# Optimization experiments

Hardware: AMD Instinct MI355X
Metric: run time of the kernel (lower is better)

Reference implementation:

```python
import jax, jax.numpy as jnp
import numpy as np

B, N, D = 4, 4096, 768
K_TOP = 8  # module's self.k
EPS = 1e-12  # F.normalize eps


def setup_inputs() -> dict:
    key = jax.random.key(0)
    k0, k1, k2 = jax.random.split(key, 3)
    s = 1.0 / np.sqrt(D)
    feats = jax.random.normal(k0, (B, N, D), dtype=jnp.float32)
    Wq = jax.random.normal(k1, (D, D), dtype=jnp.float32) * s
    bq = jnp.zeros((D,), dtype=jnp.float32)
    Wkv = jax.random.normal(k2, (D, 2 * D), dtype=jnp.float32) * s
    bkv = jnp.zeros((2 * D,), dtype=jnp.float32)
    return {"feats": feats, "Wq": Wq, "bq": bq, "Wkv": Wkv, "bkv": bkv}


def _l2norm(x):
    return x / jnp.maximum(jnp.linalg.norm(x, axis=-1, keepdims=True), EPS)


def reference(feats, Wq, bq, Wkv, bkv):
    # Only self.q and self.kv are used in the original forward; the
    # transformer encoder / norm / score_head / proj are dead code there.
    b, n, d = feats.shape
    Q = feats @ Wq + bq                      # [B,N,D]
    KV = feats @ Wkv + bkv                   # [B,N,2D]
    Kmat, Vmat = jnp.split(KV, 2, axis=-1)   # [B,N,D] each

    # cosine-distance kNN graph (self excluded via +1e6 on diagonal)
    sim = jnp.einsum('bnd,bmd->bnm', _l2norm(Q), _l2norm(Kmat))
    dist = (1.0 - sim) + jnp.eye(n, dtype=sim.dtype)[None] * 1e6
    k_eff = min(n - 1, K_TOP)
    _, idx = jax.lax.top_k(-dist, k_eff)     # smallest distances -> [B,N,k]

    # gather neighbor K/V (no O(N^2 * D) expand)
    bidx = jnp.arange(b)[:, None, None]
    Kn = Kmat[bidx, idx]                     # [B,N,k,D]
    Vn = Vmat[bidx, idx]                     # [B,N,k,D]

    attn = jnp.einsum('bnd,bnkd->bnk', Q, Kn) / np.float32(np.sqrt(d))
    attn = jax.nn.softmax(attn, axis=-1)     # [B,N,k]
    out = jnp.einsum('bnk,bnkd->bnd', attn, Vn)
    return out.mean(axis=1)                  # [B,D]
```

## Files before the change

### kernel.cpp

```cpp
#include <hip/hip_runtime.h>
#include <hip/hip_bf16.h>
#include <math.h>

#define B_ 4
#define N_ 4096
#define D_ 768
#define KTOP 8
#define M_ (B_*N_)
#define TCAND 12
#define SELK 32

typedef __attribute__((ext_vector_type(8))) short short8;
typedef __attribute__((ext_vector_type(4))) float f32x4;
typedef _Float16 half_t;
typedef __attribute__((ext_vector_type(8))) _Float16 half8;
typedef __attribute__((ext_vector_type(4))) _Float16 half4;

__device__ __forceinline__ ushort f2bf(float f) {
    unsigned int u = __float_as_uint(f);
    unsigned int r = (u + 0x7FFFu + ((u >> 16) & 1u)) >> 16;
    return (ushort)r;
}

__device__ __forceinline__ void gload16(const void* g, void* l) {
    __builtin_amdgcn_global_load_lds(
        (const __attribute__((address_space(1))) unsigned int*)g,
        (__attribute__((address_space(3))) unsigned int*)l, 16, 0, 0);
}

__global__ __launch_bounds__(256) void split_feats(
    const float* __restrict__ f, half_t* __restrict__ Fh, half_t* __restrict__ Fl)
{
    const int i = (blockIdx.x * 256 + threadIdx.x) * 4;
    const float4 v = *(const float4*)&f[i];
    float x[4] = {v.x, v.y, v.z, v.w};
    half4 h, l;
#pragma unroll
    for (int c = 0; c < 4; ++c) {
        const half_t hh = (half_t)x[c];
        h[c] = hh;
        l[c] = (half_t)(x[c] - (float)hh);
    }
    *(half4*)&Fh[i] = h;
    *(half4*)&Fl[i] = l;
}

__global__ __launch_bounds__(256) void split_w(
    const float* __restrict__ Wq, const float* __restrict__ Wkv,
    half_t* __restrict__ Wth, half_t* __restrict__ Wtl)
{
    __shared__ float T[64][65];
    const int tid = threadIdx.x;
    const int n0 = blockIdx.x * 64;
    const int k0 = blockIdx.y * 64;

    const int nl = tid & 63;
#pragma unroll
    for (int r = 0; r < 16; ++r) {
        const int kl = (tid >> 6) * 16 + r;
        const int n  = n0 + nl;
        const float w = (n < 768)
            ? Wq[(size_t)(k0 + kl) * 768 + n]
            : Wkv[(size_t)(k0 + kl) * 1536 + (n - 768)];
        T[kl][nl] = w;
    }
    __syncthreads();

    const int kl2 = tid & 63;
#pragma unroll
    for (int r = 0; r < 16; ++r) {
        const int nl2 = (tid >> 6) * 16 + r;
        const float ws = T[kl2][nl2] * 4096.0f;
        const half_t h = (half_t)ws;
        const half_t l = (half_t)(ws - (float)h);
        Wth[(size_t)(n0 + nl2) * D_ + k0 + kl2] = h;
        Wtl[(size_t)(n0 + nl2) * D_ + k0 + kl2] = l;
    }
}

__global__ __launch_bounds__(256) void qkv_mfma(
    const half_t* __restrict__ Fh, const half_t* __restrict__ Fl,
    const half_t* __restrict__ Wth, const half_t* __restrict__ Wtl,
    const float* __restrict__ bq, const float* __restrict__ bkv,
    float* __restrict__ Q, float* __restrict__ Km, float* __restrict__ Vm)
{
    __shared__ __align__(16) half_t Ah[128 * 64];
    __shared__ __align__(16) half_t Al[128 * 64];
    __shared__ __align__(16) half_t Bh[128 * 64];
    __shared__ __align__(16) half_t Bl[128 * 64];

    const int tid  = threadIdx.x;
    const int lane = tid & 63, w = tid >> 6;
    const int wr = w >> 1, wc = w & 1;
    const int r16 = lane & 15, kq = lane >> 4;
    const int n0 = blockIdx.x * 128;
    const int m0 = blockIdx.y * 128;
    const bool three = (n0 < 1536);

    const half_t* ah = Fh  + (size_t)(m0 + (tid >> 3)) * D_ + (tid & 7) * 8;
    const half_t* al = Fl  + (size_t)(m0 + (tid >> 3)) * D_ + (tid & 7) * 8;
    const half_t* bh = Wth + (size_t)(n0 + (tid >> 3)) * D_ + (tid & 7) * 8;
    const half_t* bl = Wtl + (size_t)(n0 + (tid >> 3)) * D_ + (tid & 7) * 8;
    half_t* lAh = Ah + (w << 9);
    half_t* lAl = Al + (w << 9);
    half_t* lBh = Bh + (w << 9);
    half_t* lBl = Bl + (w << 9);

    f32x4 acc[4][4];
#pragma unroll
    for (int mi = 0; mi < 4; ++mi)
#pragma unroll
        for (int ni = 0; ni < 4; ++ni) acc[mi][ni] = (f32x4)0.f;

    for (int kb = 0; kb < D_ / 64; ++kb) {
#pragma unroll
        for (int i = 0; i < 4; ++i) {
            gload16(ah + (size_t)i * 32 * D_ + kb * 64, lAh + i * 2048);
            gload16(bh + (size_t)i * 32 * D_ + kb * 64, lBh + i * 2048);
        }
        if (three) {
#pragma unroll
            for (int i = 0; i < 4; ++i) {
                gload16(al + (size_t)i * 32 * D_ + kb * 64, lAl + i * 2048);
                gload16(bl + (size_t)i * 32 * D_ + kb * 64, lBl + i * 2048);
            }
        }
        __syncthreads();
#pragma unroll
        for (int kk = 0; kk < 2; ++kk) {
            half8 fa[4], fb[4];
#pragma unroll
            for (int mi = 0; mi < 4; ++mi)
                fa[mi] = *(const half8*)&Ah[(wr * 64 + mi * 16 + r16) * 64 + kk * 32 + kq * 8];
#pragma unroll
            for (int ni = 0; ni < 4; ++ni)
                fb[ni] = *(const half8*)&Bh[(wc * 64 + ni * 16 + r16) * 64 + kk * 32 + kq * 8];
#pragma unroll
            for (int mi = 0; mi < 4; ++mi)
#pragma unroll
                for (int ni = 0; ni < 4; ++ni)
                    acc[mi][ni] = __builtin_amdgcn_mfma_f32_16x16x32_f16(
                        fa[mi], fb[ni], acc[mi][ni], 0, 0, 0);
            if (three) {
                half8 gal[4], gbl[4];
#pragma unroll
                for (int mi = 0; mi < 4; ++mi)
                    gal[mi] = *(const half8*)&Al[(wr * 64 + mi * 16 + r16) * 64 + kk * 32 + kq * 8];
#pragma unroll
                for (int ni = 0; ni < 4; ++ni)
                    gbl[ni] = *(const half8*)&Bl[(wc * 64 + ni * 16 + r16) * 64 + kk * 32 + kq * 8];
#pragma unroll
                for (int mi = 0; mi < 4; ++mi)
#pragma unroll
                    for (int ni = 0; ni < 4; ++ni) {
                        acc[mi][ni] = __builtin_amdgcn_mfma_f32_16x16x32_f16(
                            fa[mi], gbl[ni], acc[mi][ni], 0, 0, 0);
                        acc[mi][ni] = __builtin_amdgcn_mfma_f32_16x16x32_f16(
                            gal[mi], fb[ni], acc[mi][ni], 0, 0, 0);
                    }
            }
        }
        __syncthreads();
    }

    const float unscale = 1.0f / 4096.0f;
#pragma unroll
    for (int ni = 0; ni < 4; ++ni) {
        const int n = n0 + wc * 64 + ni * 16 + r16;
        const float bias = (n0 < 768) ? bq[n] : bkv[n - 768];
        float* dst; int nn;
        if      (n0 < 768)  { dst = Q;  nn = n; }
        else if (n0 < 1536) { dst = Km; nn = n - 768; }
        else                { dst = Vm; nn = n - 1536; }
#pragma unroll
        for (int mi = 0; mi < 4; ++mi)
#pragma unroll
            for (int r = 0; r < 4; ++r) {
                const int m = m0 + wr * 64 + mi * 16 + kq * 4 + r;
                dst[(size_t)m * D_ + nn] = acc[mi][ni][r] * unscale + bias;
            }
    }
}

__global__ __launch_bounds__(256) void norm_bf16(
    const float* __restrict__ Q, const float* __restrict__ Km,
    ushort* __restrict__ qn, ushort* __restrict__ kn,
    float* __restrict__ rqinv, float* __restrict__ rkinv)
{
    const int wid  = blockIdx.x * 4 + (threadIdx.x >> 6);
    const int lane = threadIdx.x & 63;
    const float* src; ushort* dst; float* rv; int r;
    if (wid < M_) { src = Q;  dst = qn; rv = rqinv; r = wid; }
    else          { src = Km; dst = kn; rv = rkinv; r = wid - M_; }
    const float* p = src + (size_t)r * D_ + lane * 12;
    float v[12];
#pragma unroll
    for (int i = 0; i < 3; ++i) *(float4*)&v[i * 4] = *(const float4*)&p[i * 4];
    float s = 0.f;
#pragma unroll
    for (int i = 0; i < 12; ++i) s += v[i] * v[i];
#pragma unroll
    for (int off = 32; off; off >>= 1) s += __shfl_xor(s, off);
    const float rinv = 1.0f / fmaxf(sqrtf(s), 1e-12f);
    ushort* op = dst + (size_t)r * D_ + lane * 12;
#pragma unroll
    for (int i = 0; i < 3; ++i) {
        ushort4 o;
        o.x = f2bf(v[i * 4 + 0] * rinv); o.y = f2bf(v[i * 4 + 1] * rinv);
        o.z = f2bf(v[i * 4 + 2] * rinv); o.w = f2bf(v[i * 4 + 3] * rinv);
        *(ushort4*)&op[i * 4] = o;
    }
    if (lane == 0) rv[r] = rinv;
}

__global__ __launch_bounds__(256) void sim_topk_fused(
    const ushort* __restrict__ qn_all, const ushort* __restrict__ kn_all,
    unsigned int* __restrict__ Part)
{
    __shared__ __align__(16) ushort smem[128 * 136];
    ushort* As = smem;
    ushort* Bs = smem + 128 * 64;

    const int tid  = threadIdx.x;
    const int lane = tid & 63, w = tid >> 6;
    const int wr = w >> 1, wc = w & 1;
    const int r16 = lane & 15, kq = lane >> 4;
    const int k0 = blockIdx.x * 128;
    const int q0 = blockIdx.y * 128;
    const int b  = blockIdx.z;

    const ushort* qsrc = qn_all + ((size_t)b * N_ + q0 + (tid >> 3)) * D_ + (tid & 7) * 8;
    const ushort* ksrc = kn_all + ((size_t)b * N_ + k0 + (tid >> 3)) * D_ + (tid & 7) * 8;
    ushort* lA = As + (w << 9);
    ushort* lB = Bs + (w << 9);

    f32x4 acc[4][4];
#pragma unroll
    for (int mi = 0; mi < 4; ++mi)
#pragma unroll
        for (int ni = 0; ni < 4; ++ni) acc[mi][ni] = (f32x4)0.f;

    for (int kb = 0; kb < D_ / 64; ++kb) {
#pragma unroll
        for (int i = 0; i < 4; ++i) {
            gload16(qsrc + (size_t)i * 32 * D_ + kb * 64, lA + i * 2048);
            gload16(ksrc + (size_t)i * 32 * D_ + kb * 64, lB + i * 2048);
        }
        __syncthreads();
#pragma unroll
        for (int kk = 0; kk < 2; ++kk) {
            short8 a[4], bfr[4];
#pragma unroll
            for (int mi = 0; mi < 4; ++mi)
                a[mi] = *(const short8*)&As[(wr * 64 + mi * 16 + r16) * 64 + kk * 32 + kq * 8];
#pragma unroll
            for (int ni = 0; ni < 4; ++ni)
                bfr[ni] = *(const short8*)&Bs[(wc * 64 + ni * 16 + r16) * 64 + kk * 32 + kq * 8];
#pragma unroll
            for (int mi = 0; mi < 4; ++mi)
#pragma unroll
                for (int ni = 0; ni < 4; ++ni)
                    acc[mi][ni] = __builtin_amdgcn_mfma_f32_16x16x32_bf16(
                        a[mi], bfr[ni], acc[mi][ni], 0, 0, 0);
        }
        __syncthreads();
    }

    ushort* St = smem;
#pragma unroll
    for (int mi = 0; mi < 4; ++mi)
#pragma unroll
        for (int ni = 0; ni < 4; ++ni)
#pragma unroll
            for (int r = 0; r < 4; ++r) {
                const int row = wr * 64 + mi * 16 + kq * 4 + r;
                const int col = wc * 64 + ni * 16 + r16;
                const bool diag = (q0 + row) == (k0 + col);
                St[row * 136 + col] = diag ? (ushort)0xFF7Fu : f2bf(acc[mi][ni][r]);
            }
    __syncthreads();

    const int rrow = tid >> 1, half = tid & 1;
    const int KREV = (N_ - 1) - (k0 + half * 64);
    const ushort* sp = St + rrow * 136 + half * 64;
    unsigned int t[TCAND];
#pragma unroll
    for (int i = 0; i < TCAND; ++i) t[i] = 0u;

#pragma unroll
    for (int j = 0; j < 64; j += 8) {
        const uint4 dv = *(const uint4*)(sp + j);
        unsigned int dw[4];
        dw[0] = dv.x; dw[1] = dv.y; dw[2] = dv.z; dw[3] = dv.w;
#pragma unroll
        for (int q = 0; q < 4; ++q) {
            const unsigned int vlo = dw[q] & 0xFFFFu;
            const unsigned int vhi = dw[q] >> 16;
            const unsigned int plo =
                ((vlo ^ (0x8000u + ((vlo >> 15) * 0x7FFFu))) << 16) |
                (unsigned int)(KREV - (j + 2 * q));
            const unsigned int phi =
                ((vhi ^ (0x8000u + ((vhi >> 15) * 0x7FFFu))) << 16) |
                (unsigned int)(KREV - (j + 2 * q + 1));
            unsigned int p = plo;
#pragma unroll
            for (int i = 0; i < TCAND; ++i) {
                const unsigned int mx = max(t[i], p);
                const unsigned int mn = min(t[i], p);
                t[i] = mx; p = mn;
            }
            p = phi;
#pragma unroll
            for (int i = 0; i < TCAND; ++i) {
                const unsigned int mx = max(t[i], p);
                const unsigned int mn = min(t[i], p);
                t[i] = mx; p = mn;
            }
        }
    }
    __syncthreads();

    unsigned int* scratch = (unsigned int*)smem;
    if (half) {
#pragma unroll
        for (int i = 0; i < TCAND; ++i) scratch[rrow * TCAND + i] = t[i];
    }
    __syncthreads();
    if (!half) {
#pragma unroll
        for (int i = 0; i < TCAND; ++i) {
            unsigned int p = scratch[rrow * TCAND + i];
#pragma unroll
            for (int s = 0; s < TCAND; ++s) {
                const unsigned int mx = max(t[s], p);
                const unsigned int mn = min(t[s], p);
                t[s] = mx; p = mn;
            }
        }
        unsigned int* op = Part +
            ((size_t)(b * N_ + q0 + rrow) * SELK + (k0 >> 7)) * TCAND;
#pragma unroll
        for (int i = 0; i < TCAND; ++i) op[i] = t[i];
    }
}

__global__ void zero_out(float* __restrict__ out)
{
    const int i = blockIdx.x * 256 + threadIdx.x;
    if (i < B_ * D_) out[i] = 0.f;
}

__global__ __launch_bounds__(256) void merge_rescore_attn(
    const float* __restrict__ Q, const float* __restrict__ Kmat,
    const float* __restrict__ Vmat, const float* __restrict__ rqinv,
    const float* __restrict__ rkinv, const unsigned int* __restrict__ Part,
    float* __restrict__ out)
{
    __shared__ float laccum[4][D_];
    const int tid  = threadIdx.x;
    const int w    = tid >> 6, lane = tid & 63;
    const int row  = blockIdx.x * 4 + w;
    const int b    = row >> 12;

    const unsigned int* pp = Part + (size_t)row * (SELK * TCAND);
    unsigned int c[6];
#pragma unroll
    for (int i = 0; i < 6; ++i) c[i] = pp[i * 64 + lane];
    unsigned int mysel = 0u;
#pragma unroll
    for (int it = 0; it < TCAND; ++it) {
        unsigned int m = c[0];
#pragma unroll
        for (int i = 1; i < 6; ++i) m = max(m, c[i]);
#pragma unroll
        for (int off = 32; off; off >>= 1) m = max(m, __shfl_xor(m, off));
#pragma unroll
        for (int i = 0; i < 6; ++i) c[i] = (c[i] == m) ? 0u : c[i];
        mysel = (lane == it) ? m : mysel;
    }
    const int kj_lane = (N_ - 1) - (int)(mysel & 0xFFFFu);

    int ka[TCAND];
#pragma unroll
    for (int j = 0; j < TCAND; ++j) ka[j] = __shfl(kj_lane, j);

    float qv[12];
    {
        const float* qp = Q + (size_t)row * D_ + lane * 12;
#pragma unroll
        for (int i = 0; i < 3; ++i) *(float4*)&qv[i * 4] = *(const float4*)&qp[i * 4];
    }
    const float rq = rqinv[row];
    const float scale = 0.03608439182435161f;

    float rkl[TCAND];
#pragma unroll
    for (int j = 0; j < TCAND; ++j) rkl[j] = rkinv[(b << 12) + ka[j]];

    float d[TCAND];
#pragma unroll
    for (int j = 0; j < TCAND; ++j) d[j] = 0.f;
#pragma unroll
    for (int j = 0; j < TCAND; ++j) {
        const float* kp = Kmat + ((size_t)(b << 12) + ka[j]) * D_ + lane * 12;
#pragma unroll
        for (int i = 0; i < 3; ++i) {
            const float4 kv = *(const float4*)&kp[i * 4];
            d[j] += qv[i * 4 + 0] * kv.x + qv[i * 4 + 1] * kv.y +
                    qv[i * 4 + 2] * kv.z + qv[i * 4 + 3] * kv.w;
        }
    }
#pragma unroll
    for (int off = 32; off; off >>= 1)
#pragma unroll
        for (int j = 0; j < TCAND; ++j) d[j] += __shfl_xor(d[j], off);

    float simv[TCAND], lgv[TCAND];
#pragma unroll
    for (int j = 0; j < TCAND; ++j) {
        simv[j] = d[j] * rq * rkl[j];
        lgv[j]  = d[j] * scale;
    }

    int rk8[TCAND];
#pragma unroll
    for (int j = 0; j < TCAND; ++j) {
        int r = 0;
#pragma unroll
        for (int o = 0; o < TCAND; ++o) {
            if (o != j)
                r += (simv[o] > simv[j] ||
                      (simv[o] == simv[j] && ka[o] < ka[j])) ? 1 : 0;
        }
        rk8[j] = r;
    }

    float mx = -1e30f;
#pragma unroll
    for (int j = 0; j < TCAND; ++j) if (rk8[j] < KTOP) mx = fmaxf(mx, lgv[j]);
    float e[TCAND]; float ps = 0.f;
#pragma unroll
    for (int j = 0; j < TCAND; ++j) {
        const float ee = (rk8[j] < KTOP) ? expf(lgv[j] - mx) : 0.f;
        e[j] = ee; ps += ee;
    }
    const float inv = 1.0f / ps;

    float oacc[12];
#pragma unroll
    for (int i = 0; i < 12; ++i) oacc[i] = 0.f;
#pragma unroll
    for (int j = 0; j < TCAND; ++j) {
        if (rk8[j] < KTOP) {
            const float p = e[j] * inv;
            const float* vp = Vmat + ((size_t)(b << 12) + ka[j]) * D_ + lane * 12;
#pragma unroll
            for (int i = 0; i < 3; ++i) {
                const float4 vv = *(const float4*)&vp[i * 4];
                oacc[i * 4 + 0] += p * vv.x; oacc[i * 4 + 1] += p * vv.y;
                oacc[i * 4 + 2] += p * vv.z; oacc[i * 4 + 3] += p * vv.w;
            }
        }
    }

#pragma unroll
    for (int i = 0; i < 3; ++i)
        *(float4*)&laccum[w][lane * 12 + i * 4] = *(float4*)&oacc[i * 4];
    __syncthreads();
    for (int dd = tid; dd < D_; dd += 256) {
        const float s = laccum[0][dd] + laccum[1][dd] + laccum[2][dd] + laccum[3][dd];
        atomicAdd(&out[(size_t)b * D_ + dd], s * (1.0f / N_));
    }
}

extern "C" void kernel_launch(void* const* d_in, const int* in_sizes, int n_in,
                              void* d_out, int out_size, void* d_ws, size_t ws_size,
                              hipStream_t stream)
{
    const float* feats = (const float*)d_in[0];
    const float* Wq    = (const float*)d_in[1];
    const float* bq    = (const float*)d_in[2];
    const float* Wkv   = (const float*)d_in[3];
    const float* bkv   = (const float*)d_in[4];
    float* out = (float*)d_out;

    char* ws = (char*)d_ws;
    size_t off = 0;
    float*  Q    = (float*)(ws + off);  off += (size_t)M_ * D_ * sizeof(float);
    float*  Km   = (float*)(ws + off);  off += (size_t)M_ * D_ * sizeof(float);
    float*  Vm   = (float*)(ws + off);  off += (size_t)M_ * D_ * sizeof(float);
    char*   unio = ws + off;            off += 2 * (size_t)M_ * D_ * sizeof(ushort);
    half_t* Fh   = (half_t*)unio;
    half_t* Fl   = (half_t*)(unio + (size_t)M_ * D_ * sizeof(half_t));
    ushort* qn   = (ushort*)unio;
    ushort* kn   = (ushort*)(unio + (size_t)M_ * D_ * sizeof(ushort));
    float*  rqv  = (float*)(ws + off);  off += (size_t)M_ * sizeof(float);
    float*  rkv  = (float*)(ws + off);  off += (size_t)M_ * sizeof(float);
    half_t* Wth  = (half_t*)(ws + off); off += (size_t)2304 * D_ * sizeof(half_t);
    half_t* Wtl  = (half_t*)(ws + off); off += (size_t)2304 * D_ * sizeof(half_t);
    unsigned int* Part = (unsigned int*)(ws + off);
    off += (size_t)M_ * SELK * TCAND * sizeof(unsigned int);
    (void)ws_size; (void)in_sizes; (void)n_in; (void)out_size;

    split_feats<<<(M_ * D_) / 1024, 256, 0, stream>>>(feats, Fh, Fl);
    split_w<<<dim3(2304 / 64, D_ / 64), 256, 0, stream>>>(Wq, Wkv, Wth, Wtl);
    qkv_mfma<<<dim3(2304 / 128, M_ / 128), 256, 0, stream>>>(
        Fh, Fl, Wth, Wtl, bq, bkv, Q, Km, Vm);
    norm_bf16<<<(2 * M_) / 4, 256, 0, stream>>>(Q, Km, qn, kn, rqv, rkv);

    sim_topk_fused<<<dim3(N_ / 128, N_ / 128, B_), 256, 0, stream>>>(qn, kn, Part);

    zero_out<<<(B_ * D_ + 255) / 256, 256, 0, stream>>>(out);
    merge_rescore_attn<<<M_ / 4, 256, 0, stream>>>(
        Q, Km, Vm, rqv, rkv, Part, out);
}
```

Measured before the change: 646.2 us.

## Store V in fp16, bitonic-merge candidates, replace atomics with partial-sum reduction

The QKV GEMM now writes V as fp16, which halves V write and gather traffic, at some precision cost on the output. The per-row candidate merge, previously twelve rounds of max-and-shuffle selection, becomes a per-lane sort followed by a cross-lane bitonic merge of 16-entry lists. Global atomicAdd accumulation is replaced by per-block partial sums written to workspace plus a separate reduce kernel, which also removes the zero_out launch. The reduce kernel adds about 12 MB of extra workspace traffic and one more launch.

```diff
diff --git a/kernel.cpp b/kernel.cpp
--- a/kernel.cpp
+++ b/kernel.cpp
@@ -28,6 +28,10 @@
         (__attribute__((address_space(3))) unsigned int*)l, 16, 0, 0);
 }
 
+#define CSD(A, i, j) { unsigned int _mx = max(A[i], A[j]); \
+                       unsigned int _mn = min(A[i], A[j]); \
+                       A[i] = _mx; A[j] = _mn; }
+
 __global__ __launch_bounds__(256) void split_feats(
     const float* __restrict__ f, half_t* __restrict__ Fh, half_t* __restrict__ Fl)
 {
@@ -82,7 +86,7 @@
     const half_t* __restrict__ Fh, const half_t* __restrict__ Fl,
     const half_t* __restrict__ Wth, const half_t* __restrict__ Wtl,
     const float* __restrict__ bq, const float* __restrict__ bkv,
-    float* __restrict__ Q, float* __restrict__ Km, float* __restrict__ Vm)
+    float* __restrict__ Q, float* __restrict__ Km, half_t* __restrict__ Vh)
 {
     __shared__ __align__(16) half_t Ah[128 * 64];
     __shared__ __align__(16) half_t Al[128 * 64];
@@ -168,17 +172,26 @@
     for (int ni = 0; ni < 4; ++ni) {
         const int n = n0 + wc * 64 + ni * 16 + r16;
         const float bias = (n0 < 768) ? bq[n] : bkv[n - 768];
-        float* dst; int nn;
-        if      (n0 < 768)  { dst = Q;  nn = n; }
-        else if (n0 < 1536) { dst = Km; nn = n - 768; }
-        else                { dst = Vm; nn = n - 1536; }
-#pragma unroll
-        for (int mi = 0; mi < 4; ++mi)
-#pragma unroll
-            for (int r = 0; r < 4; ++r) {
-                const int m = m0 + wr * 64 + mi * 16 + kq * 4 + r;
-                dst[(size_t)m * D_ + nn] = acc[mi][ni][r] * unscale + bias;
-            }
+        if (three) {
+            float* dst = (n0 < 768) ? Q : Km;
+            const int nn = (n0 < 768) ? n : (n - 768);
+#pragma unroll
+            for (int mi = 0; mi < 4; ++mi)
+#pragma unroll
+                for (int r = 0; r < 4; ++r) {
+                    const int m = m0 + wr * 64 + mi * 16 + kq * 4 + r;
+                    dst[(size_t)m * D_ + nn] = acc[mi][ni][r] * unscale + bias;
+                }
+        } else {
+            const int nn = n - 1536;
+#pragma unroll
+            for (int mi = 0; mi < 4; ++mi)
+#pragma unroll
+                for (int r = 0; r < 4; ++r) {
+                    const int m = m0 + wr * 64 + mi * 16 + kq * 4 + r;
+                    Vh[(size_t)m * D_ + nn] = (half_t)(acc[mi][ni][r] * unscale + bias);
+                }
+        }
     }
 }
 
@@ -344,17 +357,11 @@
     }
 }
 
-__global__ void zero_out(float* __restrict__ out)
-{
-    const int i = blockIdx.x * 256 + threadIdx.x;
-    if (i < B_ * D_) out[i] = 0.f;
-}
-
 __global__ __launch_bounds__(256) void merge_rescore_attn(
     const float* __restrict__ Q, const float* __restrict__ Kmat,
-    const float* __restrict__ Vmat, const float* __restrict__ rqinv,
+    const half_t* __restrict__ Vh, const float* __restrict__ rqinv,
     const float* __restrict__ rkinv, const unsigned int* __restrict__ Part,
-    float* __restrict__ out)
+    float* __restrict__ outPart)
 {
     __shared__ float laccum[4][D_];
     const int tid  = threadIdx.x;
@@ -363,26 +370,40 @@
     const int b    = row >> 12;
 
     const unsigned int* pp = Part + (size_t)row * (SELK * TCAND);
-    unsigned int c[6];
-#pragma unroll
-    for (int i = 0; i < 6; ++i) c[i] = pp[i * 64 + lane];
-    unsigned int mysel = 0u;
-#pragma unroll
-    for (int it = 0; it < TCAND; ++it) {
-        unsigned int m = c[0];
-#pragma unroll
-        for (int i = 1; i < 6; ++i) m = max(m, c[i]);
-#pragma unroll
-        for (int off = 32; off; off >>= 1) m = max(m, __shfl_xor(m, off));
-#pragma unroll
-        for (int i = 0; i < 6; ++i) c[i] = (c[i] == m) ? 0u : c[i];
-        mysel = (lane == it) ? m : mysel;
-    }
-    const int kj_lane = (N_ - 1) - (int)(mysel & 0xFFFFu);
-
+    unsigned int t[16];
+#pragma unroll
+    for (int i = 0; i < 16; ++i) t[i] = 0u;
+#pragma unroll
+    for (int i = 0; i < 6; ++i) t[i] = pp[i * 64 + lane];
+    CSD(t, 0, 5); CSD(t, 1, 3); CSD(t, 2, 4);
+    CSD(t, 1, 2); CSD(t, 3, 4);
+    CSD(t, 0, 3); CSD(t, 2, 5);
+    CSD(t, 0, 1); CSD(t, 2, 3); CSD(t, 4, 5);
+    CSD(t, 1, 2); CSD(t, 3, 4);
+#pragma unroll
+    for (int st = 0; st < 6; ++st) {
+        const int dl = 1 << st;
+        unsigned int p[16];
+#pragma unroll
+        for (int i = 0; i < 16; ++i)
+            p[i] = (unsigned int)__shfl_xor((int)t[i], dl);
+        unsigned int h[16];
+#pragma unroll
+        for (int i = 0; i < 16; ++i) h[i] = max(t[i], p[15 - i]);
+        CSD(h, 0, 8); CSD(h, 1, 9); CSD(h, 2, 10); CSD(h, 3, 11);
+        CSD(h, 4, 12); CSD(h, 5, 13); CSD(h, 6, 14); CSD(h, 7, 15);
+        CSD(h, 0, 4); CSD(h, 1, 5); CSD(h, 2, 6); CSD(h, 3, 7);
+        CSD(h, 8, 12); CSD(h, 9, 13); CSD(h, 10, 14); CSD(h, 11, 15);
+        CSD(h, 0, 2); CSD(h, 1, 3); CSD(h, 4, 6); CSD(h, 5, 7);
+        CSD(h, 8, 10); CSD(h, 9, 11); CSD(h, 12, 14); CSD(h, 13, 15);
+        CSD(h, 0, 1); CSD(h, 2, 3); CSD(h, 4, 5); CSD(h, 6, 7);
+        CSD(h, 8, 9); CSD(h, 10, 11); CSD(h, 12, 13); CSD(h, 14, 15);
+#pragma unroll
+        for (int i = 0; i < 16; ++i) t[i] = h[i];
+    }
     int ka[TCAND];
 #pragma unroll
-    for (int j = 0; j < TCAND; ++j) ka[j] = __shfl(kj_lane, j);
+    for (int j = 0; j < TCAND; ++j) ka[j] = (N_ - 1) - (int)(t[j] & 0xFFFFu);
 
     float qv[12];
     {
@@ -415,12 +436,9 @@
 #pragma unroll
         for (int j = 0; j < TCAND; ++j) d[j] += __shfl_xor(d[j], off);
 
-    float simv[TCAND], lgv[TCAND];
-#pragma unroll
-    for (int j = 0; j < TCAND; ++j) {
-        simv[j] = d[j] * rq * rkl[j];
-        lgv[j]  = d[j] * scale;
-    }
+    float simv[TCAND];
+#pragma unroll
+    for (int j = 0; j < TCAND; ++j) simv[j] = d[j] * rq * rkl[j];
 
     int rk8[TCAND];
 #pragma unroll
@@ -437,11 +455,11 @@
 
     float mx = -1e30f;
 #pragma unroll
-    for (int j = 0; j < TCAND; ++j) if (rk8[j] < KTOP) mx = fmaxf(mx, lgv[j]);
+    for (int j = 0; j < TCAND; ++j) if (rk8[j] < KTOP) mx = fmaxf(mx, d[j] * scale);
     float e[TCAND]; float ps = 0.f;
 #pragma unroll
     for (int j = 0; j < TCAND; ++j) {
-        const float ee = (rk8[j] < KTOP) ? expf(lgv[j] - mx) : 0.f;
+        const float ee = (rk8[j] < KTOP) ? expf(d[j] * scale - mx) : 0.f;
         e[j] = ee; ps += ee;
     }
     const float inv = 1.0f / ps;
@@ -453,12 +471,14 @@
     for (int j = 0; j < TCAND; ++j) {
         if (rk8[j] < KTOP) {
             const float p = e[j] * inv;
-            const float* vp = Vmat + ((size_t)(b << 12) + ka[j]) * D_ + lane * 12;
+            const half_t* vp = Vh + ((size_t)(b << 12) + ka[j]) * D_ + lane * 12;
 #pragma unroll
             for (int i = 0; i < 3; ++i) {
-                const float4 vv = *(const float4*)&vp[i * 4];
-                oacc[i * 4 + 0] += p * vv.x; oacc[i * 4 + 1] += p * vv.y;
-                oacc[i * 4 + 2] += p * vv.z; oacc[i * 4 + 3] += p * vv.w;
+                const half4 hv = *(const half4*)&vp[i * 4];
+                oacc[i * 4 + 0] += p * (float)hv[0];
+                oacc[i * 4 + 1] += p * (float)hv[1];
+                oacc[i * 4 + 2] += p * (float)hv[2];
+                oacc[i * 4 + 3] += p * (float)hv[3];
             }
         }
     }
@@ -468,9 +488,22 @@
         *(float4*)&laccum[w][lane * 12 + i * 4] = *(float4*)&oacc[i * 4];
     __syncthreads();
     for (int dd = tid; dd < D_; dd += 256) {
-        const float s = laccum[0][dd] + laccum[1][dd] + laccum[2][dd] + laccum[3][dd];
-        atomicAdd(&out[(size_t)b * D_ + dd], s * (1.0f / N_));
-    }
+        outPart[(size_t)blockIdx.x * D_ + dd] =
+            laccum[0][dd] + laccum[1][dd] + laccum[2][dd] + laccum[3][dd];
+    }
+}
+
+__global__ __launch_bounds__(256) void reduce_out(
+    const float* __restrict__ outPart, float* __restrict__ out)
+{
+    const int idx = blockIdx.x * 256 + threadIdx.x;
+    const int b = idx / D_;
+    const int dd = idx - b * D_;
+    float s = 0.f;
+#pragma unroll 8
+    for (int p = 0; p < 1024; ++p)
+        s += outPart[((size_t)(b << 10) + p) * D_ + dd];
+    out[idx] = s * (1.0f / N_);
 }
 
 extern "C" void kernel_launch(void* const* d_in, const int* in_sizes, int n_in,
@@ -488,29 +521,31 @@
     size_t off = 0;
     float*  Q    = (float*)(ws + off);  off += (size_t)M_ * D_ * sizeof(float);
     float*  Km   = (float*)(ws + off);  off += (size_t)M_ * D_ * sizeof(float);
-    float*  Vm   = (float*)(ws + off);  off += (size_t)M_ * D_ * sizeof(float);
     char*   unio = ws + off;            off += 2 * (size_t)M_ * D_ * sizeof(ushort);
     half_t* Fh   = (half_t*)unio;
     half_t* Fl   = (half_t*)(unio + (size_t)M_ * D_ * sizeof(half_t));
     ushort* qn   = (ushort*)unio;
     ushort* kn   = (ushort*)(unio + (size_t)M_ * D_ * sizeof(ushort));
+    half_t* Vh   = (half_t*)(ws + off); off += (size_t)M_ * D_ * sizeof(half_t);
     float*  rqv  = (float*)(ws + off);  off += (size_t)M_ * sizeof(float);
     float*  rkv  = (float*)(ws + off);  off += (size_t)M_ * sizeof(float);
     half_t* Wth  = (half_t*)(ws + off); off += (size_t)2304 * D_ * sizeof(half_t);
     half_t* Wtl  = (half_t*)(ws + off); off += (size_t)2304 * D_ * sizeof(half_t);
     unsigned int* Part = (unsigned int*)(ws + off);
     off += (size_t)M_ * SELK * TCAND * sizeof(unsigned int);
+    float* outPart = (float*)(ws + off);
+    off += (size_t)(M_ / 4) * D_ * sizeof(float);
     (void)ws_size; (void)in_sizes; (void)n_in; (void)out_size;
 
     split_feats<<<(M_ * D_) / 1024, 256, 0, stream>>>(feats, Fh, Fl);
     split_w<<<dim3(2304 / 64, D_ / 64), 256, 0, stream>>>(Wq, Wkv, Wth, Wtl);
     qkv_mfma<<<dim3(2304 / 128, M_ / 128), 256, 0, stream>>>(
-        Fh, Fl, Wth, Wtl, bq, bkv, Q, Km, Vm);
+        Fh, Fl, Wth, Wtl, bq, bkv, Q, Km, Vh);
     norm_bf16<<<(2 * M_) / 4, 256, 0, stream>>>(Q, Km, qn, kn, rqv, rkv);
 
     sim_topk_fused<<<dim3(N_ / 128, N_ / 128, B_), 256, 0, stream>>>(qn, kn, Part);
 
-    zero_out<<<(B_ * D_ + 255) / 256, 256, 0, stream>>>(out);
     merge_rescore_attn<<<M_ / 4, 256, 0, stream>>>(
-        Q, Km, Vm, rqv, rkv, Part, out);
-}
+        Q, Km, Vh, rqv, rkv, Part, outPart);
+    reduce_out<<<(B_ * D_) / 256, 256, 0, stream>>>(outPart, out);
+}
```

Measured after the change: 662.0 us. 1.02x slower.
